# Kernel optimization log

Hardware: AMD Instinct MI355X
Metric: run time of the kernel (lower is better)

## Reference

```python
import jax, jax.numpy as jnp
import numpy as np

B, S, DIM, NH = 2, 2048, 1536, 12
HD = DIM // NH            # 128
C = HD // 2               # 64 rotary pairs
CF = C - 2 * (C // 3)     # 22 (frame axis)
CH = C // 3               # 21 (height axis)
CW = C // 3               # 21 (width axis)
GF, GH, GW = 8, 16, 16    # grid sizes, GF*GH*GW == S
EPS = 1e-6


def _freq_table(n_pos, dim):
    inv = 1.0 / (10000.0 ** (np.arange(dim, dtype=np.float64) / dim))
    ang = np.outer(np.arange(n_pos, dtype=np.float64), inv)
    return (np.cos(ang).astype(np.float32), np.sin(ang).astype(np.float32))


def setup_inputs() -> dict:
    key = jax.random.key(0)
    ks = jax.random.split(key, 8)
    scale = 0.02
    cos_f, sin_f = _freq_table(GF, CF)
    cos_h, sin_h = _freq_table(GH, CH)
    cos_w, sin_w = _freq_table(GW, CW)
    return {
        'x': jax.random.normal(ks[0], (B, S, DIM), dtype=jnp.float32),
        'seq_lens': jnp.array([2048, 1600], dtype=jnp.int32),
        'f': GF, 'h': GH, 'w': GW,
        'wq': scale * jax.random.normal(ks[1], (DIM, DIM), dtype=jnp.float32),
        'bq': jnp.zeros((DIM,), jnp.float32),
        'wk': scale * jax.random.normal(ks[2], (DIM, DIM), dtype=jnp.float32),
        'bk': jnp.zeros((DIM,), jnp.float32),
        'wv': scale * jax.random.normal(ks[3], (DIM, DIM), dtype=jnp.float32),
        'bv': jnp.zeros((DIM,), jnp.float32),
        'wo': scale * jax.random.normal(ks[4], (DIM, DIM), dtype=jnp.float32),
        'bo': jnp.zeros((DIM,), jnp.float32),
        'nq_w': jnp.ones((DIM,), jnp.float32),
        'nk_w': jnp.ones((DIM,), jnp.float32),
        'cos_f': jnp.asarray(cos_f), 'sin_f': jnp.asarray(sin_f),
        'cos_h': jnp.asarray(cos_h), 'sin_h': jnp.asarray(sin_h),
        'cos_w': jnp.asarray(cos_w), 'sin_w': jnp.asarray(sin_w),
    }


def _rmsnorm(t, wt):
    return t * jax.lax.rsqrt(jnp.mean(t * t, axis=-1, keepdims=True) + EPS) * wt


def _grid_rope(t, cos, sin, b, s):
    # t: [b, s, NH, HD] ; cos/sin: [s, 1, C] (per-position assembled freqs)
    tp = t.reshape(b, s, NH, C, 2)
    xr, xi = tp[..., 0], tp[..., 1]
    rr = xr * cos - xi * sin          # complex multiply by e^{i*theta}
    ri = xr * sin + xi * cos
    return jnp.stack([rr, ri], axis=-1).reshape(b, s, NH, HD)


def reference(x, seq_lens, f, h, w, wq, bq, wk, bk, wv, bv, wo, bo,
              nq_w, nk_w, cos_f, sin_f, cos_h, sin_h, cos_w, sin_w):
    b, s, _ = x.shape
    # QKV projections with RMSNorm on q/k over full dim (as in the module)
    q = _rmsnorm(x @ wq.T + bq, nq_w).reshape(b, s, NH, HD)
    k = _rmsnorm(x @ wk.T + bk, nk_w).reshape(b, s, NH, HD)
    v = (x @ wv.T + bv).reshape(b, s, NH, HD)
    # grid-indexed RoPE: zero offsets / target==grid => arange sampling per axis
    idx = jnp.arange(s)
    fi = idx // (h * w)
    hi = (idx // w) % h
    wi = idx % w
    cos = jnp.concatenate([cos_f[fi], cos_h[hi], cos_w[wi]], axis=-1)[:, None, :]
    sin = jnp.concatenate([sin_f[fi], sin_h[hi], sin_w[wi]], axis=-1)[:, None, :]
    qr = _grid_rope(q, cos, sin, b, s)
    kr = _grid_rope(k, cos, sin, b, s)
    # attention with ragged key-length masking (flash_attention k_lens)
    scale = 1.0 / jnp.sqrt(jnp.float32(HD))
    scores = jnp.einsum('bqnd,bknd->bnqk', qr, kr) * scale
    kmask = idx[None, :] < seq_lens[:, None]            # [b, s]
    scores = jnp.where(kmask[:, None, None, :], scores, jnp.float32(-1e30))
    attn = jax.nn.softmax(scores, axis=-1)
    out = jnp.einsum('bnqk,bknd->bqnd', attn, v).reshape(b, s, DIM)
    return out @ wo.T + bo
```

## Files before the change

### kernel.cpp

```cpp
#include <hip/hip_runtime.h>
#include <hip/hip_bf16.h>
#include <math.h>

#define DIM_  1536
#define NH_   12
#define HD_   128
#define S_    2048
#define B_    2
#define M_    (B_*S_)
#define WEL_  (DIM_*DIM_)

typedef __attribute__((ext_vector_type(8))) _Float16 f16x8;
typedef __attribute__((ext_vector_type(4))) short short4v;
typedef __attribute__((ext_vector_type(8))) short short8v;
typedef __attribute__((ext_vector_type(4))) float f32x4;

#define SSCALE_LOG2E (0.08838834764831845f * 1.4426950408889634f)

static __device__ __forceinline__ short f2h(float f) {
  union { _Float16 h; short s; } u;
  u.h = (_Float16)f;
  return u.s;
}

static __device__ __forceinline__ unsigned pk2h(float a, float b) {
  typedef __attribute__((ext_vector_type(2))) __fp16 fp16x2;
  union { fp16x2 v; unsigned u; } u2;
  u2.v = __builtin_amdgcn_cvt_pkrtz(a, b);
  return u2.u;
}

__global__ __launch_bounds__(256) void f2h5_k(
    const float* __restrict__ x, const float* __restrict__ wq,
    const float* __restrict__ wk, const float* __restrict__ wv,
    const float* __restrict__ wo,
    short* __restrict__ x16, short* __restrict__ w16, short* __restrict__ wo16)
{
  int i = blockIdx.x * 256 + threadIdx.x;
  const float* src; short* dst; int j;
  if (i < 786432)       { src = x;  dst = x16;            j = i; }
  else if (i < 1081344) { src = wq; dst = w16;            j = i - 786432; }
  else if (i < 1376256) { src = wk; dst = w16 + WEL_;     j = i - 1081344; }
  else if (i < 1671168) { src = wv; dst = w16 + 2 * WEL_; j = i - 1376256; }
  else                  { src = wo; dst = wo16;           j = i - 1671168; }
  const float4* p = (const float4*)src + (size_t)j * 2;
  float4 a = p[0], b = p[1];
  short8v o;
  o[0] = f2h(a.x); o[1] = f2h(a.y); o[2] = f2h(a.z); o[3] = f2h(a.w);
  o[4] = f2h(b.x); o[5] = f2h(b.y); o[6] = f2h(b.z); o[7] = f2h(b.w);
  *((short8v*)dst + j) = o;
}

template<int MODE>
static __device__ __forceinline__ void gemm16_core(
    const short* __restrict__ A16, const short* __restrict__ W16,
    const float* __restrict__ bias, short* __restrict__ Outp,
    int m0, int n0, char* __restrict__ Ab, char* __restrict__ Bb)
{
  const int tid = threadIdx.x;
  const int l  = tid & 63, w = tid >> 6;
  const int wr = w >> 1, wc = w & 1;
  const int lc = l & 15, lg = l >> 4;

  f32x4 acc[4][4] = {};

  const int rs  = w * 16 + (l >> 2);
  const int gsl = ((l & 3) ^ ((rs >> 1) & 3)) * 8;
  const short* gA0 = A16 + (size_t)(m0 + rs) * DIM_ + gsl;
  const short* gA1 = A16 + (size_t)(m0 + 64 + rs) * DIM_ + gsl;
  const short* gB0 = W16 + (size_t)(n0 + rs) * DIM_ + gsl;
  const short* gB1 = W16 + (size_t)(n0 + 64 + rs) * DIM_ + gsl;

#define GSTAGE(buf, k0)                                                        \
  {                                                                            \
    __builtin_amdgcn_global_load_lds(                                          \
        (const __attribute__((address_space(1))) unsigned*)(gA0 + (k0)),       \
        (__attribute__((address_space(3))) unsigned*)(Ab + (buf) * 8192 + w * 1024), 16, 0, 0); \
    __builtin_amdgcn_global_load_lds(                                          \
        (const __attribute__((address_space(1))) unsigned*)(gA1 + (k0)),       \
        (__attribute__((address_space(3))) unsigned*)(Ab + (buf) * 8192 + 4096 + w * 1024), 16, 0, 0); \
    __builtin_amdgcn_global_load_lds(                                          \
        (const __attribute__((address_space(1))) unsigned*)(gB0 + (k0)),       \
        (__attribute__((address_space(3))) unsigned*)(Bb + (buf) * 8192 + w * 1024), 16, 0, 0); \
    __builtin_amdgcn_global_load_lds(                                          \
        (const __attribute__((address_space(1))) unsigned*)(gB1 + (k0)),       \
        (__attribute__((address_space(3))) unsigned*)(Bb + (buf) * 8192 + 4096 + w * 1024), 16, 0, 0); \
  }

  GSTAGE(0, 0);
  __syncthreads();
  int cur = 0;
  for (int k0 = 0; k0 < DIM_; k0 += 32) {
    const char* Ac = Ab + cur * 8192;
    const char* Bc = Bb + cur * 8192;
    f16x8 af[4], bf[4];
#pragma unroll
    for (int mt = 0; mt < 4; ++mt) {
      int ar = wr * 64 + mt * 16 + lc;
      af[mt] = *(const f16x8*)(Ac + ar * 64 + ((lg ^ ((ar >> 1) & 3)) << 4));
    }
#pragma unroll
    for (int nt = 0; nt < 4; ++nt) {
      int br = wc * 64 + nt * 16 + lc;
      bf[nt] = *(const f16x8*)(Bc + br * 64 + ((lg ^ ((br >> 1) & 3)) << 4));
    }
    if (k0 + 32 < DIM_) GSTAGE(cur ^ 1, k0 + 32);
    __builtin_amdgcn_s_setprio(1);
#pragma unroll
    for (int mt = 0; mt < 4; ++mt)
#pragma unroll
      for (int nt = 0; nt < 4; ++nt)
        acc[mt][nt] = __builtin_amdgcn_mfma_f32_16x16x32_f16(af[mt], bf[nt], acc[mt][nt], 0, 0, 0);
    __builtin_amdgcn_s_setprio(0);
    __syncthreads();
    cur ^= 1;
  }
#undef GSTAGE

  if (MODE == 0) {
#pragma unroll
    for (int nt = 0; nt < 4; ++nt) {
      int col = n0 + wc * 64 + nt * 16 + lc;
      float bb = bias[col];
#pragma unroll
      for (int mt = 0; mt < 4; ++mt) {
#pragma unroll
        for (int r = 0; r < 4; ++r) {
          int rowm = m0 + wr * 64 + mt * 16 + lg * 4 + r;
          Outp[(size_t)rowm * DIM_ + col] = f2h(acc[mt][nt][r] + bb);
        }
      }
    }
  } else {
#pragma unroll
    for (int nt = 0; nt < 4; ++nt) {
      int colg = n0 + wc * 64 + nt * 16 + lc;
      int h = colg >> 7, d = colg & 127;
      float bb = bias[colg];
#pragma unroll
      for (int mt = 0; mt < 4; ++mt) {
        int rowg = m0 + wr * 64 + mt * 16 + lg * 4;
        int b = rowg >> 11, s = rowg & (S_ - 1);
        short4v o4;
#pragma unroll
        for (int r = 0; r < 4; ++r) o4[r] = f2h(acc[mt][nt][r] + bb);
        *(short4v*)(Outp + ((size_t)((b * NH_ + h) * HD_ + d)) * S_ + s) = o4;
      }
    }
  }
}

__global__ __launch_bounds__(256) void gemm_qkv16_k(
    const short* __restrict__ x16, const short* __restrict__ w16,
    const float* __restrict__ bq, const float* __restrict__ bk,
    const float* __restrict__ bv,
    short* __restrict__ q16, short* __restrict__ k16, short* __restrict__ vt)
{
  __shared__ __align__(16) char Ab[2][8192];
  __shared__ __align__(16) char Bb[2][8192];
  const int z = blockIdx.z;
  if (z == 2)
    gemm16_core<2>(x16, w16 + 2 * (size_t)WEL_, bv, vt,
                   blockIdx.y * 128, blockIdx.x * 128, &Ab[0][0], &Bb[0][0]);
  else
    gemm16_core<0>(x16, w16 + (size_t)z * WEL_, z ? bk : bq, z ? k16 : q16,
                   blockIdx.y * 128, blockIdx.x * 128, &Ab[0][0], &Bb[0][0]);
}

__global__ __launch_bounds__(256) void gemm_out64_k(
    const short* __restrict__ att16, const short* __restrict__ wo16,
    const float* __restrict__ bo, float* __restrict__ out)
{
  __shared__ __align__(16) char Ab[2][8192];
  __shared__ __align__(16) char Bb[2][4096];
  const int m0 = blockIdx.y * 128, n0 = blockIdx.x * 64;
  const int tid = threadIdx.x;
  const int l  = tid & 63, w = tid >> 6;
  const int lc = l & 15, lg = l >> 4;

  f32x4 acc[2][4] = {};

  const int rsA = w * 32 + (l >> 2);
  const int rsB = w * 16 + (l >> 2);
  const int gslA = ((l & 3) ^ ((rsA >> 1) & 3)) * 8;
  const int gslB = ((l & 3) ^ ((rsB >> 1) & 3)) * 8;
  const short* gA0 = att16 + (size_t)(m0 + rsA) * DIM_ + gslA;
  const short* gA1 = att16 + (size_t)(m0 + 16 + rsA) * DIM_ + gslA;
  const short* gB0 = wo16 + (size_t)(n0 + rsB) * DIM_ + gslB;

#define GSTAGE(buf, k0)                                                        \
  {                                                                            \
    __builtin_amdgcn_global_load_lds(                                          \
        (const __attribute__((address_space(1))) unsigned*)(gA0 + (k0)),       \
        (__attribute__((address_space(3))) unsigned*)(&Ab[buf][0] + w * 2048), 16, 0, 0); \
    __builtin_amdgcn_global_load_lds(                                          \
        (const __attribute__((address_space(1))) unsigned*)(gA1 + (k0)),       \
        (__attribute__((address_space(3))) unsigned*)(&Ab[buf][0] + w * 2048 + 1024), 16, 0, 0); \
    __builtin_amdgcn_global_load_lds(                                          \
        (const __attribute__((address_space(1))) unsigned*)(gB0 + (k0)),       \
        (__attribute__((address_space(3))) unsigned*)(&Bb[buf][0] + w * 1024), 16, 0, 0); \
  }

  GSTAGE(0, 0);
  __syncthreads();
  int cur = 0;
  for (int k0 = 0; k0 < DIM_; k0 += 32) {
    const char* Ac = &Ab[cur][0];
    const char* Bc = &Bb[cur][0];
    f16x8 af[2], bf[4];
#pragma unroll
    for (int mt = 0; mt < 2; ++mt) {
      int ar = w * 32 + mt * 16 + lc;
      af[mt] = *(const f16x8*)(Ac + ar * 64 + ((lg ^ ((ar >> 1) & 3)) << 4));
    }
#pragma unroll
    for (int nt = 0; nt < 4; ++nt) {
      int br = nt * 16 + lc;
      bf[nt] = *(const f16x8*)(Bc + br * 64 + ((lg ^ ((br >> 1) & 3)) << 4));
    }
    if (k0 + 32 < DIM_) GSTAGE(cur ^ 1, k0 + 32);
    __builtin_amdgcn_s_setprio(1);
#pragma unroll
    for (int mt = 0; mt < 2; ++mt)
#pragma unroll
      for (int nt = 0; nt < 4; ++nt)
        acc[mt][nt] = __builtin_amdgcn_mfma_f32_16x16x32_f16(af[mt], bf[nt], acc[mt][nt], 0, 0, 0);
    __builtin_amdgcn_s_setprio(0);
    __syncthreads();
    cur ^= 1;
  }
#undef GSTAGE

#pragma unroll
  for (int nt = 0; nt < 4; ++nt) {
    int col = n0 + nt * 16 + lc;
    float bb = bo[col];
#pragma unroll
    for (int mt = 0; mt < 2; ++mt) {
#pragma unroll
      for (int r = 0; r < 4; ++r) {
        int rowm = m0 + w * 32 + mt * 16 + lg * 4 + r;
        out[(size_t)rowm * DIM_ + col] = acc[mt][nt][r] + bb;
      }
    }
  }
}

__global__ __launch_bounds__(256) void rms_rope_qk_k(
    const short* __restrict__ q16, const short* __restrict__ k16,
    const float* __restrict__ nq, const float* __restrict__ nk,
    const float* __restrict__ cf, const float* __restrict__ sf,
    const float* __restrict__ ch, const float* __restrict__ sh,
    const float* __restrict__ cw, const float* __restrict__ sw,
    short* __restrict__ qh, short* __restrict__ kh)
{
  const int z   = blockIdx.y;
  const short* t = z ? k16 : q16;
  const float* w = z ? nk : nq;
  short* outb   = z ? kh : qh;
  const float qsc0 = z ? 1.0f : SSCALE_LOG2E;

  const int row = blockIdx.x;
  const int b   = row >> 11;
  const int s   = row & (S_ - 1);
  const _Float16* rp = (const _Float16*)(t + (size_t)row * DIM_);

  float ss = 0.f;
  for (int i = threadIdx.x; i < DIM_; i += 256) {
    float v2 = (float)rp[i]; ss += v2 * v2;
  }
#pragma unroll
  for (int off = 32; off > 0; off >>= 1) ss += __shfl_down(ss, off);
  __shared__ float red[4];
  if ((threadIdx.x & 63) == 0) red[threadIdx.x >> 6] = ss;
  __syncthreads();
  float scale = rsqrtf((red[0] + red[1] + red[2] + red[3]) * (1.f / DIM_) + 1e-6f) * qsc0;

  const int fi = s >> 8;
  const int hi = (s >> 4) & 15;
  const int wi = s & 15;

  for (int p = threadIdx.x; p < NH_ * 64; p += 256) {
    int n = p >> 6, c = p & 63;
    float co, si;
    if (c < 22)      { co = cf[fi * 22 + c];        si = sf[fi * 22 + c]; }
    else if (c < 43) { co = ch[hi * 21 + (c - 22)]; si = sh[hi * 21 + (c - 22)]; }
    else             { co = cw[wi * 21 + (c - 43)]; si = sw[wi * 21 + (c - 43)]; }
    int d0 = n * HD_ + 2 * c;
    float xr = (float)rp[d0]     * scale * w[d0];
    float xi = (float)rp[d0 + 1] * scale * w[d0 + 1];
    float rr = xr * co - xi * si;
    float ri = xr * si + xi * co;
    *(unsigned int*)(outb + (((size_t)(b * NH_ + n) * S_ + s) * HD_ + 2 * c)) = pk2h(rr, ri);
  }
}

__global__ __launch_bounds__(256) void attn_mfma5_k(
    const short* __restrict__ qb, const short* __restrict__ kb,
    const short* __restrict__ vtb, const int* __restrict__ seq_lens,
    short* __restrict__ o16)
{
  const int bh = blockIdx.y;
  const int b  = bh / NH_;
  const int h  = bh - b * NH_;
  const int q0 = blockIdx.x << 6;
  const int kvlen = seq_lens[b];
  const int tid  = threadIdx.x;
  const int wid  = tid >> 6;
  const int lane = tid & 63;
  const int lg   = lane >> 4;
  const int lc   = lane & 15;
  const int xo   = (lc & 7) << 4;

  __shared__ __align__(16) char Kt[16384];
  __shared__ __align__(16) char Vt[16384];
  __shared__ __align__(16) char Pt[4][2048];

  f16x8 bq[4];
  {
    const size_t base = ((size_t)bh * S_ + q0 + wid * 16 + lc) * HD_;
#pragma unroll
    for (int dc = 0; dc < 4; ++dc)
      bq[dc] = *(const f16x8*)(qb + base + dc * 32 + lg * 8);
  }

  const short* kgA = kb + ((size_t)bh * S_ + wid * 16 + lg) * HD_
                        + ((lc * 8) ^ (lg << 3));
  const short* kgB = kb + ((size_t)bh * S_ + wid * 16 + 4 + lg) * HD_
                        + ((lc * 8) ^ ((lg ^ 4) << 3));
  const short* vg  = vtb + ((size_t)bh * HD_ + wid * 32 + (lane >> 3)) * S_
                         + (((lane & 7) * 8) ^ ((lane >> 3) << 3));

#define STAGE_K()                                                              \
  {                                                                            \
    _Pragma("unroll")                                                          \
    for (int j = 0; j < 4; ++j) {                                              \
      const short* g = (j & 1) ? (kgB + ((j - 1) >> 1) * (8 * HD_))            \
                               : (kgA + (j >> 1) * (8 * HD_));                 \
      __builtin_amdgcn_global_load_lds(                                        \
          (const __attribute__((address_space(1))) unsigned*)g,                \
          (__attribute__((address_space(3))) unsigned*)(Kt + (wid * 16 + j * 4) * 256), \
          16, 0, 0);                                                           \
    }                                                                          \
  }
#define STAGE_V()                                                              \
  {                                                                            \
    _Pragma("unroll")                                                          \
    for (int j = 0; j < 4; ++j) {                                              \
      __builtin_amdgcn_global_load_lds(                                        \
          (const __attribute__((address_space(1))) unsigned*)(vg + j * 8 * S_),\
          (__attribute__((address_space(3))) unsigned*)(Vt + (wid * 32 + j * 8) * 128), \
          16, 0, 0);                                                           \
    }                                                                          \
  }

  f32x4 oacc[8] = {};
  float m = -3.0e38f, l = 0.f;

  const int nt = kvlen >> 6;

  STAGE_K();
  kgA += 64 * HD_; kgB += 64 * HD_;
  __syncthreads();

  for (int ti = 0; ti < nt; ++ti) {
    STAGE_V();
    vg += 64;

    f32x4 s[4];
    __builtin_amdgcn_s_setprio(1);
#pragma unroll
    for (int kt = 0; kt < 4; ++kt) {
      f32x4 a = {0.f, 0.f, 0.f, 0.f};
      const char* kr = Kt + (kt * 16 + lc) * 256;
#pragma unroll
      for (int dc = 0; dc < 4; ++dc) {
        f16x8 kf = *(const f16x8*)(kr + ((dc * 64 + lg * 16) ^ xo));
        a = __builtin_amdgcn_mfma_f32_16x16x32_f16(kf, bq[dc], a, 0, 0, 0);
      }
      s[kt] = a;
    }
    __builtin_amdgcn_s_setprio(0);

    float t0 = -3.0e38f;
#pragma unroll
    for (int kt = 0; kt < 4; ++kt)
#pragma unroll
      for (int r = 0; r < 4; ++r) t0 = fmaxf(t0, s[kt][r]);
    t0 = fmaxf(t0, __shfl_xor(t0, 16));
    t0 = fmaxf(t0, __shfl_xor(t0, 32));

    if (__any(t0 > m + 8.f)) {
      float mn = fmaxf(m, t0);
      float a  = exp2f(m - mn);
      m = mn; l *= a;
#pragma unroll
      for (int r = 0; r < 4; ++r) {
        float ar = __shfl(a, 4 * lg + r);
#pragma unroll
        for (int n = 0; n < 8; ++n) oacc[n][r] *= ar;
      }
    }
    float ls = 0.f;
#pragma unroll
    for (int kt = 0; kt < 4; ++kt)
#pragma unroll
      for (int r = 0; r < 4; ++r) {
        float p = exp2f(s[kt][r] - m); s[kt][r] = p; ls += p;
      }
    ls += __shfl_xor(ls, 16);
    ls += __shfl_xor(ls, 32);
    l += ls;

    {
      char* pr = Pt[wid] + lc * 128;
#pragma unroll
      for (int kt = 0; kt < 4; ++kt) {
#pragma unroll
        for (int rr = 0; rr < 2; ++rr) {
          unsigned u = pk2h(s[kt][2 * rr], s[kt][2 * rr + 1]);
          int off = (kt * 32 + lg * 8 + rr * 4) ^ xo;
          *(unsigned*)(pr + off) = u;
        }
      }
    }

    __syncthreads();

    if (ti + 1 < nt) {
      STAGE_K();
      kgA += 64 * HD_; kgB += 64 * HD_;
    }

    __builtin_amdgcn_s_setprio(1);
#pragma unroll
    for (int kc = 0; kc < 2; ++kc) {
      f16x8 pa = *(const f16x8*)(Pt[wid] + lc * 128 + ((kc * 64 + lg * 16) ^ xo));
#pragma unroll
      for (int n = 0; n < 8; ++n) {
        f16x8 vf = *(const f16x8*)(Vt + (n * 16 + lc) * 128 + ((kc * 64 + lg * 16) ^ xo));
        oacc[n] = __builtin_amdgcn_mfma_f32_16x16x32_f16(pa, vf, oacc[n], 0, 0, 0);
      }
    }
    __builtin_amdgcn_s_setprio(0);

    __syncthreads();
  }

#pragma unroll
  for (int r = 0; r < 4; ++r) {
    float li = 1.f / __shfl(l, 4 * lg + r);
    int qrow = q0 + wid * 16 + 4 * lg + r;
#pragma unroll
    for (int n = 0; n < 8; ++n)
      o16[((size_t)(b * S_ + qrow) * NH_ + h) * HD_ + n * 16 + lc] = f2h(oacc[n][r] * li);
  }
#undef STAGE_K
#undef STAGE_V
}

extern "C" void kernel_launch(void* const* d_in, const int* in_sizes, int n_in,
                              void* d_out, int out_size, void* d_ws, size_t ws_size,
                              hipStream_t stream) {
  const float* x        = (const float*)d_in[0];
  const int*   seq_lens = (const int*)d_in[1];
  const float* wq = (const float*)d_in[5];
  const float* bq = (const float*)d_in[6];
  const float* wk = (const float*)d_in[7];
  const float* bk = (const float*)d_in[8];
  const float* wv = (const float*)d_in[9];
  const float* bv = (const float*)d_in[10];
  const float* wo = (const float*)d_in[11];
  const float* bo = (const float*)d_in[12];
  const float* nq = (const float*)d_in[13];
  const float* nk = (const float*)d_in[14];
  const float* cf = (const float*)d_in[15];
  const float* sf = (const float*)d_in[16];
  const float* ch = (const float*)d_in[17];
  const float* sh = (const float*)d_in[18];
  const float* cw = (const float*)d_in[19];
  const float* sw = (const float*)d_in[20];

  const size_t rowelems = (size_t)M_ * DIM_;
  short* x16  = (short*)d_ws;
  short* w16  = x16 + rowelems;
  short* wo16 = w16 + 3 * (size_t)WEL_;
  short* q16  = wo16 + WEL_;
  short* k16  = q16 + rowelems;
  short* vt   = k16 + rowelems;
  short* qh   = vt + rowelems;
  short* kh   = qh + rowelems;
  short* att16 = q16;
  float* out = (float*)d_out;

  f2h5_k<<<7680, 256, 0, stream>>>(x, wq, wk, wv, wo, x16, w16, wo16);

  gemm_qkv16_k<<<dim3(DIM_ / 128, M_ / 128, 3), 256, 0, stream>>>(
      x16, w16, bq, bk, bv, q16, k16, vt);

  rms_rope_qk_k<<<dim3(M_, 2), 256, 0, stream>>>(
      q16, k16, nq, nk, cf, sf, ch, sh, cw, sw, qh, kh);

  attn_mfma5_k<<<dim3(S_ / 64, B_ * NH_), 256, 0, stream>>>(qh, kh, vt, seq_lens, att16);

  gemm_out64_k<<<dim3(DIM_ / 64, M_ / 128), 256, 0, stream>>>(att16, wo16, bo, out);
}
```

Before: 246.6 us.

## Triple-buffer GEMM LDS staging with one barrier per k-step and vmcnt waits

Both the QKV and output projection GEMMs move from double-buffered LDS staging with two __syncthreads per iteration to a three-stage ring. Global-to-LDS loads are issued two k-steps ahead, and a partial s_waitcnt vmcnt plus a single s_barrier gates each step. This is meant to hide more global load latency and cut synchronization stalls. The cost is 1.5x the LDS per block, which may lower occupancy, and the hand-written waitcnt counts must match the number of loads issued per stage.

After: 261.9 us. 6.2% more time.

```diff
diff --git a/kernel.cpp b/kernel.cpp
--- a/kernel.cpp
+++ b/kernel.cpp
@@ -87,35 +87,53 @@
         (__attribute__((address_space(3))) unsigned*)(Bb + (buf) * 8192 + 4096 + w * 1024), 16, 0, 0); \
   }
 
+#define FRAGMFMA(bufidx)                                                       \
+  {                                                                            \
+    const char* Ac = Ab + (bufidx) * 8192;                                     \
+    const char* Bc = Bb + (bufidx) * 8192;                                     \
+    f16x8 af[4], bf[4];                                                        \
+    _Pragma("unroll")                                                          \
+    for (int mt = 0; mt < 4; ++mt) {                                           \
+      int ar = wr * 64 + mt * 16 + lc;                                         \
+      af[mt] = *(const f16x8*)(Ac + ar * 64 + ((lg ^ ((ar >> 1) & 3)) << 4));  \
+    }                                                                          \
+    _Pragma("unroll")                                                          \
+    for (int nt = 0; nt < 4; ++nt) {                                           \
+      int br = wc * 64 + nt * 16 + lc;                                         \
+      bf[nt] = *(const f16x8*)(Bc + br * 64 + ((lg ^ ((br >> 1) & 3)) << 4));  \
+    }                                                                          \
+    __builtin_amdgcn_s_setprio(1);                                             \
+    _Pragma("unroll")                                                          \
+    for (int mt = 0; mt < 4; ++mt)                                             \
+      _Pragma("unroll")                                                        \
+      for (int nt = 0; nt < 4; ++nt)                                           \
+        acc[mt][nt] = __builtin_amdgcn_mfma_f32_16x16x32_f16(af[mt], bf[nt], acc[mt][nt], 0, 0, 0); \
+    __builtin_amdgcn_s_setprio(0);                                             \
+  }
+
   GSTAGE(0, 0);
-  __syncthreads();
+  GSTAGE(1, 32);
   int cur = 0;
-  for (int k0 = 0; k0 < DIM_; k0 += 32) {
-    const char* Ac = Ab + cur * 8192;
-    const char* Bc = Bb + cur * 8192;
-    f16x8 af[4], bf[4];
-#pragma unroll
-    for (int mt = 0; mt < 4; ++mt) {
-      int ar = wr * 64 + mt * 16 + lc;
-      af[mt] = *(const f16x8*)(Ac + ar * 64 + ((lg ^ ((ar >> 1) & 3)) << 4));
-    }
-#pragma unroll
-    for (int nt = 0; nt < 4; ++nt) {
-      int br = wc * 64 + nt * 16 + lc;
-      bf[nt] = *(const f16x8*)(Bc + br * 64 + ((lg ^ ((br >> 1) & 3)) << 4));
-    }
-    if (k0 + 32 < DIM_) GSTAGE(cur ^ 1, k0 + 32);
-    __builtin_amdgcn_s_setprio(1);
-#pragma unroll
-    for (int mt = 0; mt < 4; ++mt)
-#pragma unroll
-      for (int nt = 0; nt < 4; ++nt)
-        acc[mt][nt] = __builtin_amdgcn_mfma_f32_16x16x32_f16(af[mt], bf[nt], acc[mt][nt], 0, 0, 0);
-    __builtin_amdgcn_s_setprio(0);
-    __syncthreads();
-    cur ^= 1;
-  }
+  for (int k0 = 0; k0 < DIM_ - 64; k0 += 32) {
+    asm volatile("s_waitcnt vmcnt(4)" ::: "memory");
+    __builtin_amdgcn_s_barrier();
+    __builtin_amdgcn_sched_barrier(0);
+    int nb = cur + 2; if (nb >= 3) nb -= 3;
+    GSTAGE(nb, k0 + 64);
+    FRAGMFMA(cur);
+    ++cur; if (cur >= 3) cur = 0;
+  }
+  asm volatile("s_waitcnt vmcnt(4)" ::: "memory");
+  __builtin_amdgcn_s_barrier();
+  __builtin_amdgcn_sched_barrier(0);
+  FRAGMFMA(cur);
+  ++cur; if (cur >= 3) cur = 0;
+  asm volatile("s_waitcnt vmcnt(0)" ::: "memory");
+  __builtin_amdgcn_s_barrier();
+  __builtin_amdgcn_sched_barrier(0);
+  FRAGMFMA(cur);
 #undef GSTAGE
+#undef FRAGMFMA
 
   if (MODE == 0) {
 #pragma unroll
@@ -156,23 +174,23 @@
     const float* __restrict__ bv,
     short* __restrict__ q16, short* __restrict__ k16, short* __restrict__ vt)
 {
-  __shared__ __align__(16) char Ab[2][8192];
-  __shared__ __align__(16) char Bb[2][8192];
+  __shared__ __align__(16) char Ab[3 * 8192];
+  __shared__ __align__(16) char Bb[3 * 8192];
   const int z = blockIdx.z;
   if (z == 2)
     gemm16_core<2>(x16, w16 + 2 * (size_t)WEL_, bv, vt,
-                   blockIdx.y * 128, blockIdx.x * 128, &Ab[0][0], &Bb[0][0]);
+                   blockIdx.y * 128, blockIdx.x * 128, Ab, Bb);
   else
     gemm16_core<0>(x16, w16 + (size_t)z * WEL_, z ? bk : bq, z ? k16 : q16,
-                   blockIdx.y * 128, blockIdx.x * 128, &Ab[0][0], &Bb[0][0]);
+                   blockIdx.y * 128, blockIdx.x * 128, Ab, Bb);
 }
 
 __global__ __launch_bounds__(256) void gemm_out64_k(
     const short* __restrict__ att16, const short* __restrict__ wo16,
     const float* __restrict__ bo, float* __restrict__ out)
 {
-  __shared__ __align__(16) char Ab[2][8192];
-  __shared__ __align__(16) char Bb[2][4096];
+  __shared__ __align__(16) char Ab[3 * 8192];
+  __shared__ __align__(16) char Bb[3 * 4096];
   const int m0 = blockIdx.y * 128, n0 = blockIdx.x * 64;
   const int tid = threadIdx.x;
   const int l  = tid & 63, w = tid >> 6;
@@ -192,44 +210,62 @@
   {                                                                            \
     __builtin_amdgcn_global_load_lds(                                          \
         (const __attribute__((address_space(1))) unsigned*)(gA0 + (k0)),       \
-        (__attribute__((address_space(3))) unsigned*)(&Ab[buf][0] + w * 2048), 16, 0, 0); \
+        (__attribute__((address_space(3))) unsigned*)(Ab + (buf) * 8192 + w * 2048), 16, 0, 0); \
     __builtin_amdgcn_global_load_lds(                                          \
         (const __attribute__((address_space(1))) unsigned*)(gA1 + (k0)),       \
-        (__attribute__((address_space(3))) unsigned*)(&Ab[buf][0] + w * 2048 + 1024), 16, 0, 0); \
+        (__attribute__((address_space(3))) unsigned*)(Ab + (buf) * 8192 + w * 2048 + 1024), 16, 0, 0); \
     __builtin_amdgcn_global_load_lds(                                          \
         (const __attribute__((address_space(1))) unsigned*)(gB0 + (k0)),       \
-        (__attribute__((address_space(3))) unsigned*)(&Bb[buf][0] + w * 1024), 16, 0, 0); \
+        (__attribute__((address_space(3))) unsigned*)(Bb + (buf) * 4096 + w * 1024), 16, 0, 0); \
+  }
+
+#define FRAGMFMA(bufidx)                                                       \
+  {                                                                            \
+    const char* Ac = Ab + (bufidx) * 8192;                                     \
+    const char* Bc = Bb + (bufidx) * 4096;                                     \
+    f16x8 af[2], bf[4];                                                        \
+    _Pragma("unroll")                                                          \
+    for (int mt = 0; mt < 2; ++mt) {                                           \
+      int ar = w * 32 + mt * 16 + lc;                                          \
+      af[mt] = *(const f16x8*)(Ac + ar * 64 + ((lg ^ ((ar >> 1) & 3)) << 4));  \
+    }                                                                          \
+    _Pragma("unroll")                                                          \
+    for (int nt = 0; nt < 4; ++nt) {                                           \
+      int br = nt * 16 + lc;                                                   \
+      bf[nt] = *(const f16x8*)(Bc + br * 64 + ((lg ^ ((br >> 1) & 3)) << 4));  \
+    }                                                                          \
+    __builtin_amdgcn_s_setprio(1);                                             \
+    _Pragma("unroll")                                                          \
+    for (int mt = 0; mt < 2; ++mt)                                             \
+      _Pragma("unroll")                                                        \
+      for (int nt = 0; nt < 4; ++nt)                                           \
+        acc[mt][nt] = __builtin_amdgcn_mfma_f32_16x16x32_f16(af[mt], bf[nt], acc[mt][nt], 0, 0, 0); \
+    __builtin_amdgcn_s_setprio(0);                                             \
   }
 
   GSTAGE(0, 0);
-  __syncthreads();
+  GSTAGE(1, 32);
   int cur = 0;
-  for (int k0 = 0; k0 < DIM_; k0 += 32) {
-    const char* Ac = &Ab[cur][0];
-    const char* Bc = &Bb[cur][0];
-    f16x8 af[2], bf[4];
-#pragma unroll
-    for (int mt = 0; mt < 2; ++mt) {
-      int ar = w * 32 + mt * 16 + lc;
-      af[mt] = *(const f16x8*)(Ac + ar * 64 + ((lg ^ ((ar >> 1) & 3)) << 4));
-    }
-#pragma unroll
-    for (int nt = 0; nt < 4; ++nt) {
-      int br = nt * 16 + lc;
-      bf[nt] = *(const f16x8*)(Bc + br * 64 + ((lg ^ ((br >> 1) & 3)) << 4));
-    }
-    if (k0 + 32 < DIM_) GSTAGE(cur ^ 1, k0 + 32);
-    __builtin_amdgcn_s_setprio(1);
-#pragma unroll
-    for (int mt = 0; mt < 2; ++mt)
-#pragma unroll
-      for (int nt = 0; nt < 4; ++nt)
-        acc[mt][nt] = __builtin_amdgcn_mfma_f32_16x16x32_f16(af[mt], bf[nt], acc[mt][nt], 0, 0, 0);
-    __builtin_amdgcn_s_setprio(0);
-    __syncthreads();
-    cur ^= 1;
-  }
+  for (int k0 = 0; k0 < DIM_ - 64; k0 += 32) {
+    asm volatile("s_waitcnt vmcnt(3)" ::: "memory");
+    __builtin_amdgcn_s_barrier();
+    __builtin_amdgcn_sched_barrier(0);
+    int nb = cur + 2; if (nb >= 3) nb -= 3;
+    GSTAGE(nb, k0 + 64);
+    FRAGMFMA(cur);
+    ++cur; if (cur >= 3) cur = 0;
+  }
+  asm volatile("s_waitcnt vmcnt(3)" ::: "memory");
+  __builtin_amdgcn_s_barrier();
+  __builtin_amdgcn_sched_barrier(0);
+  FRAGMFMA(cur);
+  ++cur; if (cur >= 3) cur = 0;
+  asm volatile("s_waitcnt vmcnt(0)" ::: "memory");
+  __builtin_amdgcn_s_barrier();
+  __builtin_amdgcn_sched_barrier(0);
+  FRAGMFMA(cur);
 #undef GSTAGE
+#undef FRAGMFMA
 
 #pragma unroll
   for (int nt = 0; nt < 4; ++nt) {
```

## Process two 16-row query tiles per wave to reuse K/V tiles in attention

Applied to the files above, without the earlier changes.

The attention kernel now covers 128 query rows per block, with each wave handling two 16-row query tiles. Each wave keeps separate max, sum and output accumulators per tile, while the staged K and V tiles in shared memory are shared across both. This halves the K/V global-to-LDS traffic per query and doubles MFMA work per LDS fragment read. The cost is more registers per wave, a larger P buffer in shared memory, and half as many blocks, which may hurt occupancy and load balance across CUs.

New measurement: 254.5 us. 1.03x slower.

```diff
diff --git a/kernel.cpp b/kernel.cpp
--- a/kernel.cpp
+++ b/kernel.cpp
@@ -295,7 +295,7 @@
   }
 }
 
-__global__ __launch_bounds__(256) void attn_mfma5_k(
+__global__ __launch_bounds__(256) void attn_mfma6_k(
     const short* __restrict__ qb, const short* __restrict__ kb,
     const short* __restrict__ vtb, const int* __restrict__ seq_lens,
     short* __restrict__ o16)
@@ -303,7 +303,7 @@
   const int bh = blockIdx.y;
   const int b  = bh / NH_;
   const int h  = bh - b * NH_;
-  const int q0 = blockIdx.x << 6;
+  const int q0 = blockIdx.x << 7;
   const int kvlen = seq_lens[b];
   const int tid  = threadIdx.x;
   const int wid  = tid >> 6;
@@ -314,14 +314,16 @@
 
   __shared__ __align__(16) char Kt[16384];
   __shared__ __align__(16) char Vt[16384];
-  __shared__ __align__(16) char Pt[4][2048];
-
-  f16x8 bq[4];
+  __shared__ __align__(16) char Pt[4][4096];
+
+  f16x8 bq0[4], bq1[4];
   {
-    const size_t base = ((size_t)bh * S_ + q0 + wid * 16 + lc) * HD_;
-#pragma unroll
-    for (int dc = 0; dc < 4; ++dc)
-      bq[dc] = *(const f16x8*)(qb + base + dc * 32 + lg * 8);
+    const size_t base = ((size_t)bh * S_ + q0 + wid * 32 + lc) * HD_;
+#pragma unroll
+    for (int dc = 0; dc < 4; ++dc) {
+      bq0[dc] = *(const f16x8*)(qb + base + dc * 32 + lg * 8);
+      bq1[dc] = *(const f16x8*)(qb + base + 16 * HD_ + dc * 32 + lg * 8);
+    }
   }
 
   const short* kgA = kb + ((size_t)bh * S_ + wid * 16 + lg) * HD_
@@ -354,8 +356,8 @@
     }                                                                          \
   }
 
-  f32x4 oacc[8] = {};
-  float m = -3.0e38f, l = 0.f;
+  f32x4 oacc0[8] = {}, oacc1[8] = {};
+  float m0 = -3.0e38f, m1 = -3.0e38f, l0 = 0.f, l1 = 0.f;
 
   const int nt = kvlen >> 6;
 
@@ -367,60 +369,67 @@
     STAGE_V();
     vg += 64;
 
-    f32x4 s[4];
+    f32x4 s0[4], s1[4];
     __builtin_amdgcn_s_setprio(1);
 #pragma unroll
     for (int kt = 0; kt < 4; ++kt) {
-      f32x4 a = {0.f, 0.f, 0.f, 0.f};
+      f32x4 a0 = {0.f, 0.f, 0.f, 0.f}, a1 = {0.f, 0.f, 0.f, 0.f};
       const char* kr = Kt + (kt * 16 + lc) * 256;
 #pragma unroll
       for (int dc = 0; dc < 4; ++dc) {
         f16x8 kf = *(const f16x8*)(kr + ((dc * 64 + lg * 16) ^ xo));
-        a = __builtin_amdgcn_mfma_f32_16x16x32_f16(kf, bq[dc], a, 0, 0, 0);
-      }
-      s[kt] = a;
+        a0 = __builtin_amdgcn_mfma_f32_16x16x32_f16(kf, bq0[dc], a0, 0, 0, 0);
+        a1 = __builtin_amdgcn_mfma_f32_16x16x32_f16(kf, bq1[dc], a1, 0, 0, 0);
+      }
+      s0[kt] = a0; s1[kt] = a1;
     }
     __builtin_amdgcn_s_setprio(0);
 
-    float t0 = -3.0e38f;
+    float t0 = -3.0e38f, t1 = -3.0e38f;
 #pragma unroll
     for (int kt = 0; kt < 4; ++kt)
 #pragma unroll
-      for (int r = 0; r < 4; ++r) t0 = fmaxf(t0, s[kt][r]);
-    t0 = fmaxf(t0, __shfl_xor(t0, 16));
-    t0 = fmaxf(t0, __shfl_xor(t0, 32));
-
-    if (__any(t0 > m + 8.f)) {
-      float mn = fmaxf(m, t0);
-      float a  = exp2f(m - mn);
-      m = mn; l *= a;
-#pragma unroll
       for (int r = 0; r < 4; ++r) {
-        float ar = __shfl(a, 4 * lg + r);
-#pragma unroll
-        for (int n = 0; n < 8; ++n) oacc[n][r] *= ar;
-      }
-    }
-    float ls = 0.f;
+        t0 = fmaxf(t0, s0[kt][r]); t1 = fmaxf(t1, s1[kt][r]);
+      }
+    t0 = fmaxf(t0, __shfl_xor(t0, 16)); t0 = fmaxf(t0, __shfl_xor(t0, 32));
+    t1 = fmaxf(t1, __shfl_xor(t1, 16)); t1 = fmaxf(t1, __shfl_xor(t1, 32));
+
+    if (__any((t0 > m0 + 8.f) || (t1 > m1 + 8.f))) {
+      float mn0 = fmaxf(m0, t0), mn1 = fmaxf(m1, t1);
+      float a0 = exp2f(m0 - mn0), a1 = exp2f(m1 - mn1);
+      m0 = mn0; m1 = mn1; l0 *= a0; l1 *= a1;
+#pragma unroll
+      for (int r = 0; r < 4; ++r) {
+        float ar0 = __shfl(a0, 4 * lg + r);
+        float ar1 = __shfl(a1, 4 * lg + r);
+#pragma unroll
+        for (int n = 0; n < 8; ++n) { oacc0[n][r] *= ar0; oacc1[n][r] *= ar1; }
+      }
+    }
+    float ls0 = 0.f, ls1 = 0.f;
 #pragma unroll
     for (int kt = 0; kt < 4; ++kt)
 #pragma unroll
       for (int r = 0; r < 4; ++r) {
-        float p = exp2f(s[kt][r] - m); s[kt][r] = p; ls += p;
-      }
-    ls += __shfl_xor(ls, 16);
-    ls += __shfl_xor(ls, 32);
-    l += ls;
+        float p0 = exp2f(s0[kt][r] - m0); s0[kt][r] = p0; ls0 += p0;
+        float p1 = exp2f(s1[kt][r] - m1); s1[kt][r] = p1; ls1 += p1;
+      }
+    ls0 += __shfl_xor(ls0, 16); ls0 += __shfl_xor(ls0, 32); l0 += ls0;
+    ls1 += __shfl_xor(ls1, 16); ls1 += __shfl_xor(ls1, 32); l1 += ls1;
 
     {
-      char* pr = Pt[wid] + lc * 128;
+      char* pr0 = Pt[wid] + lc * 128;
+      char* pr1 = Pt[wid] + (16 + lc) * 128;
 #pragma unroll
       for (int kt = 0; kt < 4; ++kt) {
 #pragma unroll
         for (int rr = 0; rr < 2; ++rr) {
-          unsigned u = pk2h(s[kt][2 * rr], s[kt][2 * rr + 1]);
+          unsigned u0 = pk2h(s0[kt][2 * rr], s0[kt][2 * rr + 1]);
+          unsigned u1 = pk2h(s1[kt][2 * rr], s1[kt][2 * rr + 1]);
           int off = (kt * 32 + lg * 8 + rr * 4) ^ xo;
-          *(unsigned*)(pr + off) = u;
+          *(unsigned*)(pr0 + off) = u0;
+          *(unsigned*)(pr1 + off) = u1;
         }
       }
     }
@@ -435,11 +444,13 @@
     __builtin_amdgcn_s_setprio(1);
 #pragma unroll
     for (int kc = 0; kc < 2; ++kc) {
-      f16x8 pa = *(const f16x8*)(Pt[wid] + lc * 128 + ((kc * 64 + lg * 16) ^ xo));
+      f16x8 pa0 = *(const f16x8*)(Pt[wid] + lc * 128 + ((kc * 64 + lg * 16) ^ xo));
+      f16x8 pa1 = *(const f16x8*)(Pt[wid] + (16 + lc) * 128 + ((kc * 64 + lg * 16) ^ xo));
 #pragma unroll
       for (int n = 0; n < 8; ++n) {
         f16x8 vf = *(const f16x8*)(Vt + (n * 16 + lc) * 128 + ((kc * 64 + lg * 16) ^ xo));
-        oacc[n] = __builtin_amdgcn_mfma_f32_16x16x32_f16(pa, vf, oacc[n], 0, 0, 0);
+        oacc0[n] = __builtin_amdgcn_mfma_f32_16x16x32_f16(pa0, vf, oacc0[n], 0, 0, 0);
+        oacc1[n] = __builtin_amdgcn_mfma_f32_16x16x32_f16(pa1, vf, oacc1[n], 0, 0, 0);
       }
     }
     __builtin_amdgcn_s_setprio(0);
@@ -449,11 +460,14 @@
 
 #pragma unroll
   for (int r = 0; r < 4; ++r) {
-    float li = 1.f / __shfl(l, 4 * lg + r);
-    int qrow = q0 + wid * 16 + 4 * lg + r;
-#pragma unroll
-    for (int n = 0; n < 8; ++n)
-      o16[((size_t)(b * S_ + qrow) * NH_ + h) * HD_ + n * 16 + lc] = f2h(oacc[n][r] * li);
+    float li0 = 1.f / __shfl(l0, 4 * lg + r);
+    float li1 = 1.f / __shfl(l1, 4 * lg + r);
+    int qrow = q0 + wid * 32 + 4 * lg + r;
+#pragma unroll
+    for (int n = 0; n < 8; ++n) {
+      o16[((size_t)(b * S_ + qrow) * NH_ + h) * HD_ + n * 16 + lc] = f2h(oacc0[n][r] * li0);
+      o16[((size_t)(b * S_ + qrow + 16) * NH_ + h) * HD_ + n * 16 + lc] = f2h(oacc1[n][r] * li1);
+    }
   }
 #undef STAGE_K
 #undef STAGE_V
@@ -501,7 +515,7 @@
   rms_rope_qk_k<<<dim3(M_, 2), 256, 0, stream>>>(
       q16, k16, nq, nk, cf, sf, ch, sh, cw, sw, qh, kh);
 
-  attn_mfma5_k<<<dim3(S_ / 64, B_ * NH_), 256, 0, stream>>>(qh, kh, vt, seq_lens, att16);
+  attn_mfma6_k<<<dim3(S_ / 128, B_ * NH_), 256, 0, stream>>>(qh, kh, vt, seq_lens, att16);
 
   gemm_out64_k<<<dim3(DIM_ / 64, M_ / 128), 256, 0, stream>>>(att16, wo16, bo, out);
 }
```
